# Kernel tuning notes

Hardware: AMD Instinct MI355X
Metric: run time of the kernel (lower is better)

Reference implementation:

```python
import jax, jax.numpy as jnp
import numpy as np

N_NODES = 50000
N_EDGES = 800000
IN_FEATS = 128
OUT_FEATS = 128
N_REL = 3


def setup_inputs() -> dict:
    key = jax.random.key(0)
    k1, k2, k3, k4, k5, k6 = jax.random.split(key, 6)
    feature = jax.random.normal(k1, (N_NODES, IN_FEATS), dtype=jnp.float32)
    # kaiming_uniform-ish scale for faithfulness of magnitude
    bound = float(np.sqrt(6.0 / IN_FEATS))
    weight = jax.random.uniform(k2, (N_REL, IN_FEATS, OUT_FEATS), dtype=jnp.float32,
                                minval=-bound, maxval=bound)
    norm = jax.random.uniform(k3, (N_EDGES,), dtype=jnp.float32)
    src = jax.random.randint(k4, (N_EDGES,), 0, N_NODES)
    dst = jax.random.randint(k5, (N_EDGES,), 0, N_NODES)
    rel_type = jax.random.randint(k6, (N_EDGES,), 0, N_REL)
    return {"feature": feature, "weight": weight, "norm": norm,
            "src": src, "dst": dst, "rel_type": rel_type}


def reference(feature, weight, norm, src, dst, rel_type):
    # Per-edge message: norm_e * (x[src_e] @ W[rel_type_e]).
    # Since there are only 3 relations, transform ALL nodes once per relation
    # (grouped GEMM: [3, N, in] x [3, in, out]) then gather the right
    # (relation, src) row per edge -- same math, avoids per-edge bmm.
    hr = jnp.einsum('ni,rio->rno', feature, weight)       # [3, N, out]
    msg = hr[rel_type, src] * norm[:, None]               # [E, out]
    # fn.sum reduce -> scatter-sum into destination nodes (zero if no in-edges)
    h = jax.ops.segment_sum(msg, dst, num_segments=feature.shape[0])  # [N, out]
    return jax.nn.relu(h)
```

## Files before the change

kernel.cpp:

```cpp
#include <hip/hip_runtime.h>
#include <stdint.h>

#define NFEAT  128
#define NREL   3

typedef short short8 __attribute__((ext_vector_type(8)));
typedef float f32x4  __attribute__((ext_vector_type(4)));

__device__ __forceinline__ uint32_t f2bf(float x) {
    uint32_t u = __builtin_bit_cast(uint32_t, x);
    uint32_t r = (u + 0x7FFFu + ((u >> 16) & 1u)) >> 16;
    return r & 0xFFFFu;
}
__device__ __forceinline__ float bf2f(uint32_t b) {
    uint32_t u = b << 16;
    return __builtin_bit_cast(float, u);
}

__global__ __launch_bounds__(256) void k_prep_w(
    const float* __restrict__ W, uint16_t* __restrict__ Wt, int* __restrict__ bincnt)
{
    const int tid = blockIdx.x * 256 + threadIdx.x;
    if (blockIdx.x == 0) bincnt[threadIdx.x] = 0;
    if (tid >= NREL * NFEAT * 16) return;
    const int k8 = tid & 15;
    const int o  = (tid >> 4) & 127;
    const int r  = tid >> 11;
    const float* Wr = W + (size_t)r * NFEAT * NFEAT;
    uint32_t pk[4];
    #pragma unroll
    for (int q = 0; q < 4; q++) {
        float lo = Wr[(size_t)(k8 * 8 + q * 2)     * NFEAT + o];
        float hi = Wr[(size_t)(k8 * 8 + q * 2 + 1) * NFEAT + o];
        pk[q] = f2bf(lo) | (f2bf(hi) << 16);
    }
    uint4 v = make_uint4(pk[0], pk[1], pk[2], pk[3]);
    *reinterpret_cast<uint4*>(&Wt[(size_t)r * NFEAT * NFEAT + (size_t)o * NFEAT + k8 * 8]) = v;
}

__global__ __launch_bounds__(256) void k_gemm_mfma(
    const float* __restrict__ feat, const uint16_t* __restrict__ Wt,
    uint16_t* __restrict__ hr, int N)
{
    __shared__ uint16_t ldsA[64 * 128];
    __shared__ uint16_t ldsB[128 * 128];

    const int t    = threadIdx.x;
    const int lane = t & 63;
    const int w    = t >> 6;
    const int n0   = blockIdx.x * 64;

    {
        const int kq = t & 15;
        const int rq = t >> 4;
        #pragma unroll
        for (int rr = 0; rr < 4; rr++) {
            const int row = rr * 16 + rq;
            const int n = n0 + row;
            uint4 pk = make_uint4(0, 0, 0, 0);
            if (n < N) {
                const float4* p = reinterpret_cast<const float4*>(&feat[(size_t)n * NFEAT + kq * 8]);
                float4 v0 = p[0], v1 = p[1];
                pk.x = f2bf(v0.x) | (f2bf(v0.y) << 16);
                pk.y = f2bf(v0.z) | (f2bf(v0.w) << 16);
                pk.z = f2bf(v1.x) | (f2bf(v1.y) << 16);
                pk.w = f2bf(v1.z) | (f2bf(v1.w) << 16);
            }
            uint32_t byte = (uint32_t)(row * 256 + kq * 16) ^ ((uint32_t)(row & 7) << 4);
            *reinterpret_cast<uint4*>(reinterpret_cast<char*>(ldsA) + byte) = pk;
        }
    }

    const int rowf = lane & 15;
    const int kb   = lane >> 4;

    for (int r = 0; r < NREL; r++) {
        {
            const int kq = t & 15;
            const int rq = t >> 4;
            const uint16_t* Wr = Wt + (size_t)r * NFEAT * NFEAT;
            #pragma unroll
            for (int rr = 0; rr < 8; rr++) {
                const int row = rr * 16 + rq;
                uint4 v = *reinterpret_cast<const uint4*>(&Wr[(size_t)row * NFEAT + kq * 8]);
                uint32_t byte = (uint32_t)(row * 256 + kq * 16) ^ ((uint32_t)(row & 7) << 4);
                *reinterpret_cast<uint4*>(reinterpret_cast<char*>(ldsB) + byte) = v;
            }
        }
        __syncthreads();

        short8 a[4];
        {
            const int row = w * 16 + rowf;
            #pragma unroll
            for (int ks = 0; ks < 4; ks++) {
                uint32_t byte = (uint32_t)(row * 256 + ks * 64 + kb * 16) ^ ((uint32_t)(row & 7) << 4);
                a[ks] = *reinterpret_cast<const short8*>(reinterpret_cast<char*>(ldsA) + byte);
            }
        }

        f32x4 acc[8];
        #pragma unroll
        for (int cf = 0; cf < 8; cf++) acc[cf] = (f32x4){0.f, 0.f, 0.f, 0.f};

        #pragma unroll
        for (int cf = 0; cf < 8; cf++) {
            const int col = cf * 16 + rowf;
            #pragma unroll
            for (int ks = 0; ks < 4; ks++) {
                uint32_t byte = (uint32_t)(col * 256 + ks * 64 + kb * 16) ^ ((uint32_t)(col & 7) << 4);
                short8 b = *reinterpret_cast<const short8*>(reinterpret_cast<char*>(ldsB) + byte);
                acc[cf] = __builtin_amdgcn_mfma_f32_16x16x32_bf16(a[ks], b, acc[cf], 0, 0, 0);
            }
        }

        #pragma unroll
        for (int cf = 0; cf < 8; cf++) {
            #pragma unroll
            for (int j = 0; j < 4; j++) {
                const int n = n0 + w * 16 + kb * 4 + j;
                if (n < N)
                    hr[((size_t)r * N + n) * NFEAT + cf * 16 + rowf] = (uint16_t)f2bf(acc[cf][j]);
            }
        }
        __syncthreads();
    }
}

__global__ __launch_bounds__(256) void k_binhist(
    const int* __restrict__ dst, int* __restrict__ bincnt, int E)
{
    __shared__ int h[256];
    const int t = threadIdx.x;
    h[t] = 0;
    __syncthreads();
    int e = blockIdx.x * 2048 + t;
    #pragma unroll
    for (int j = 0; j < 8; j++, e += 256)
        if (e < E) atomicAdd(&h[dst[e] >> 8], 1);
    __syncthreads();
    if (h[t]) atomicAdd(&bincnt[t], h[t]);
}

__global__ __launch_bounds__(256) void k_binscan(
    const int* __restrict__ bincnt, int* __restrict__ binoff,
    int* __restrict__ bincursor, int* __restrict__ offsets,
    int N, int E, int nbins)
{
    __shared__ int sm[256];
    const int t = threadIdx.x;
    int v = (t < nbins) ? bincnt[t] : 0;
    sm[t] = v;
    __syncthreads();
    for (int s = 1; s < 256; s <<= 1) {
        int a = (t >= s) ? sm[t - s] : 0;
        __syncthreads();
        sm[t] += a;
        __syncthreads();
    }
    int excl = sm[t] - v;
    if (t < nbins) { binoff[t] = excl; bincursor[t] = excl; }
    if (t == 0) { binoff[nbins] = E; offsets[N] = E; }
}

__global__ __launch_bounds__(256) void k_binfill(
    const int* __restrict__ dst, const int* __restrict__ src,
    const int* __restrict__ rel, const float* __restrict__ norm,
    int* __restrict__ bincursor, uint2* __restrict__ binbuf, int E)
{
    __shared__ int hist[256];
    __shared__ int base[256];
    __shared__ int rank[256];
    const int t = threadIdx.x;
    const int e0 = blockIdx.x * 2048;

    hist[t] = 0;
    __syncthreads();

    int myBin[8], myDl[8];
    #pragma unroll
    for (int j = 0; j < 8; j++) {
        int e = e0 + t + j * 256;
        int b = -1, dl = 0;
        if (e < E) {
            int d = dst[e];
            b = d >> 8;
            dl = d & 255;
            atomicAdd(&hist[b], 1);
        }
        myBin[j] = b;
        myDl[j] = dl;
    }
    __syncthreads();

    int h = hist[t];
    if (h > 0) base[t] = atomicAdd(&bincursor[t], h);
    rank[t] = 0;
    __syncthreads();

    #pragma unroll
    for (int j = 0; j < 8; j++) {
        int e = e0 + t + j * 256;
        if (myBin[j] >= 0) {
            int p = base[myBin[j]] + atomicAdd(&rank[myBin[j]], 1);
            uint32_t px = (uint32_t)src[e] | ((uint32_t)rel[e] << 16) | ((uint32_t)myDl[j] << 18);
            binbuf[p] = make_uint2(px, __builtin_bit_cast(uint32_t, norm[e]));
        }
    }
}

__global__ __launch_bounds__(256) void k_binsort(
    const uint2* __restrict__ binbuf, const int* __restrict__ binoff,
    uint2* __restrict__ meta, int* __restrict__ offsets, int N)
{
    __shared__ int sm[256];
    __shared__ int cur[256];
    const int b = blockIdx.x;
    const int t = threadIdx.x;
    const int base = binoff[b];
    const int cnt  = binoff[b + 1] - base;

    sm[t] = 0;
    __syncthreads();
    for (int i = t; i < cnt; i += 256) {
        uint2 r = binbuf[base + i];
        atomicAdd(&sm[(r.x >> 18) & 255], 1);
    }
    __syncthreads();
    int v = sm[t];
    __syncthreads();
    sm[t] = v;
    __syncthreads();
    for (int s = 1; s < 256; s <<= 1) {
        int a = (t >= s) ? sm[t - s] : 0;
        __syncthreads();
        sm[t] += a;
        __syncthreads();
    }
    int excl = sm[t] - v;
    int n = b * 256 + t;
    if (n < N) offsets[n] = base + excl;
    cur[t] = excl;
    __syncthreads();

    for (int i = t; i < cnt; i += 256) {
        uint2 r = binbuf[base + i];
        int dl = (r.x >> 18) & 255;
        int p = atomicAdd(&cur[dl], 1);
        meta[base + p] = make_uint2(r.x & 0x3FFFFu, r.y);
    }
}

__global__ __launch_bounds__(256) void k_aggregate(
    const uint16_t* __restrict__ hr, const int* __restrict__ offsets,
    const uint2* __restrict__ meta, float* __restrict__ out, int N)
{
    const int wid  = threadIdx.x >> 6;
    const int lane = threadIdx.x & 63;
    const int n = blockIdx.x * 4 + wid;
    if (n >= N) return;

    const int start = offsets[n];
    const int end   = offsets[n + 1];
    const int c = lane * 2;

    float a0 = 0.f, a1 = 0.f, b0 = 0.f, b1 = 0.f;
    int idx = start;

    for (; idx + 7 < end; idx += 8) {
        uint2 m[8];
        #pragma unroll
        for (int j = 0; j < 8; j++) m[j] = meta[idx + j];
        uint32_t v[8];
        #pragma unroll
        for (int j = 0; j < 8; j++)
            v[j] = *reinterpret_cast<const uint32_t*>(
                &hr[((size_t)(m[j].x >> 16) * N + (m[j].x & 0xFFFFu)) * NFEAT + c]);
        #pragma unroll
        for (int j = 0; j < 8; j += 2) {
            float w0 = __builtin_bit_cast(float, m[j].y);
            float w1 = __builtin_bit_cast(float, m[j + 1].y);
            a0 += w0 * bf2f(v[j] & 0xFFFFu);     a1 += w0 * bf2f(v[j] >> 16);
            b0 += w1 * bf2f(v[j + 1] & 0xFFFFu); b1 += w1 * bf2f(v[j + 1] >> 16);
        }
    }
    for (; idx + 3 < end; idx += 4) {
        uint2 m[4];
        #pragma unroll
        for (int j = 0; j < 4; j++) m[j] = meta[idx + j];
        uint32_t v[4];
        #pragma unroll
        for (int j = 0; j < 4; j++)
            v[j] = *reinterpret_cast<const uint32_t*>(
                &hr[((size_t)(m[j].x >> 16) * N + (m[j].x & 0xFFFFu)) * NFEAT + c]);
        #pragma unroll
        for (int j = 0; j < 4; j += 2) {
            float w0 = __builtin_bit_cast(float, m[j].y);
            float w1 = __builtin_bit_cast(float, m[j + 1].y);
            a0 += w0 * bf2f(v[j] & 0xFFFFu);     a1 += w0 * bf2f(v[j] >> 16);
            b0 += w1 * bf2f(v[j + 1] & 0xFFFFu); b1 += w1 * bf2f(v[j + 1] >> 16);
        }
    }
    for (; idx < end; idx++) {
        uint2 m = meta[idx];
        uint32_t v = *reinterpret_cast<const uint32_t*>(
            &hr[((size_t)(m.x >> 16) * N + (m.x & 0xFFFFu)) * NFEAT + c]);
        float wgt = __builtin_bit_cast(float, m.y);
        a0 += wgt * bf2f(v & 0xFFFFu);
        a1 += wgt * bf2f(v >> 16);
    }

    float2 o;
    o.x = fmaxf(a0 + b0, 0.f);
    o.y = fmaxf(a1 + b1, 0.f);
    *reinterpret_cast<float2*>(&out[(size_t)n * NFEAT + c]) = o;
}

extern "C" void kernel_launch(void* const* d_in, const int* in_sizes, int n_in,
                              void* d_out, int out_size, void* d_ws, size_t ws_size,
                              hipStream_t stream)
{
    const float* feat = (const float*)d_in[0];
    const float* W    = (const float*)d_in[1];
    const float* norm = (const float*)d_in[2];
    const int*   src  = (const int*)d_in[3];
    const int*   dst  = (const int*)d_in[4];
    const int*   rel  = (const int*)d_in[5];
    float* out = (float*)d_out;

    const int N = in_sizes[0] / NFEAT;
    const int E = in_sizes[2];
    const int NBINS = (N + 255) / 256;
    const int HB = (E + 2047) / 2048;

    char* ws = (char*)d_ws;
    size_t off = 0;
    auto alloc = [&](size_t bytes) -> char* {
        char* p = ws + off;
        off += (bytes + 63) & ~(size_t)63;
        return p;
    };
    uint16_t* hr    = (uint16_t*)alloc((size_t)NREL * N * NFEAT * 2);
    uint16_t* Wt    = (uint16_t*)alloc((size_t)NREL * NFEAT * NFEAT * 2);
    int* bincnt     = (int*)alloc(256 * 4);
    int* binoff     = (int*)alloc(257 * 4);
    int* bincursor  = (int*)alloc(256 * 4);
    int* offsets    = (int*)alloc((size_t)(N + 1) * 4);
    uint2* meta     = (uint2*)alloc((size_t)E * 8);
    (void)ws_size;

    uint2* binbuf = (uint2*)d_out;

    k_prep_w<<<(NREL * NFEAT * 16 + 255) / 256, 256, 0, stream>>>(W, Wt, bincnt);
    k_gemm_mfma<<<(N + 63) / 64, 256, 0, stream>>>(feat, Wt, hr, N);
    k_binhist<<<HB, 256, 0, stream>>>(dst, bincnt, E);
    k_binscan<<<1, 256, 0, stream>>>(bincnt, binoff, bincursor, offsets, N, E, NBINS);
    k_binfill<<<HB, 256, 0, stream>>>(dst, src, rel, norm, bincursor, binbuf, E);
    k_binsort<<<NBINS, 256, 0, stream>>>(binbuf, binoff, meta, offsets, N);
    k_aggregate<<<(N + 3) / 4, 256, 0, stream>>>(hr, offsets, meta, out, N);
}
```

Measured before the change: 107.4 us.

## Aggregate raw features per relation before the weight GEMM

```diff
diff --git a/kernel.cpp b/kernel.cpp
--- a/kernel.cpp
+++ b/kernel.cpp
@@ -17,150 +17,83 @@
     return __builtin_bit_cast(float, u);
 }
 
-__global__ __launch_bounds__(256) void k_prep_w(
-    const float* __restrict__ W, uint16_t* __restrict__ Wt, int* __restrict__ bincnt)
-{
-    const int tid = blockIdx.x * 256 + threadIdx.x;
-    if (blockIdx.x == 0) bincnt[threadIdx.x] = 0;
-    if (tid >= NREL * NFEAT * 16) return;
-    const int k8 = tid & 15;
-    const int o  = (tid >> 4) & 127;
-    const int r  = tid >> 11;
-    const float* Wr = W + (size_t)r * NFEAT * NFEAT;
-    uint32_t pk[4];
-    #pragma unroll
-    for (int q = 0; q < 4; q++) {
-        float lo = Wr[(size_t)(k8 * 8 + q * 2)     * NFEAT + o];
-        float hi = Wr[(size_t)(k8 * 8 + q * 2 + 1) * NFEAT + o];
-        pk[q] = f2bf(lo) | (f2bf(hi) << 16);
-    }
-    uint4 v = make_uint4(pk[0], pk[1], pk[2], pk[3]);
-    *reinterpret_cast<uint4*>(&Wt[(size_t)r * NFEAT * NFEAT + (size_t)o * NFEAT + k8 * 8]) = v;
-}
-
-__global__ __launch_bounds__(256) void k_gemm_mfma(
-    const float* __restrict__ feat, const uint16_t* __restrict__ Wt,
-    uint16_t* __restrict__ hr, int N)
-{
-    __shared__ uint16_t ldsA[64 * 128];
-    __shared__ uint16_t ldsB[128 * 128];
-
-    const int t    = threadIdx.x;
-    const int lane = t & 63;
-    const int w    = t >> 6;
-    const int n0   = blockIdx.x * 64;
-
-    {
-        const int kq = t & 15;
-        const int rq = t >> 4;
-        #pragma unroll
-        for (int rr = 0; rr < 4; rr++) {
-            const int row = rr * 16 + rq;
-            const int n = n0 + row;
-            uint4 pk = make_uint4(0, 0, 0, 0);
-            if (n < N) {
-                const float4* p = reinterpret_cast<const float4*>(&feat[(size_t)n * NFEAT + kq * 8]);
-                float4 v0 = p[0], v1 = p[1];
-                pk.x = f2bf(v0.x) | (f2bf(v0.y) << 16);
-                pk.y = f2bf(v0.z) | (f2bf(v0.w) << 16);
-                pk.z = f2bf(v1.x) | (f2bf(v1.y) << 16);
-                pk.w = f2bf(v1.z) | (f2bf(v1.w) << 16);
-            }
-            uint32_t byte = (uint32_t)(row * 256 + kq * 16) ^ ((uint32_t)(row & 7) << 4);
-            *reinterpret_cast<uint4*>(reinterpret_cast<char*>(ldsA) + byte) = pk;
-        }
-    }
-
-    const int rowf = lane & 15;
-    const int kb   = lane >> 4;
-
-    for (int r = 0; r < NREL; r++) {
-        {
-            const int kq = t & 15;
-            const int rq = t >> 4;
-            const uint16_t* Wr = Wt + (size_t)r * NFEAT * NFEAT;
-            #pragma unroll
-            for (int rr = 0; rr < 8; rr++) {
-                const int row = rr * 16 + rq;
-                uint4 v = *reinterpret_cast<const uint4*>(&Wr[(size_t)row * NFEAT + kq * 8]);
-                uint32_t byte = (uint32_t)(row * 256 + kq * 16) ^ ((uint32_t)(row & 7) << 4);
-                *reinterpret_cast<uint4*>(reinterpret_cast<char*>(ldsB) + byte) = v;
-            }
-        }
-        __syncthreads();
-
-        short8 a[4];
-        {
-            const int row = w * 16 + rowf;
-            #pragma unroll
-            for (int ks = 0; ks < 4; ks++) {
-                uint32_t byte = (uint32_t)(row * 256 + ks * 64 + kb * 16) ^ ((uint32_t)(row & 7) << 4);
-                a[ks] = *reinterpret_cast<const short8*>(reinterpret_cast<char*>(ldsA) + byte);
-            }
-        }
-
-        f32x4 acc[8];
-        #pragma unroll
-        for (int cf = 0; cf < 8; cf++) acc[cf] = (f32x4){0.f, 0.f, 0.f, 0.f};
-
-        #pragma unroll
-        for (int cf = 0; cf < 8; cf++) {
-            const int col = cf * 16 + rowf;
-            #pragma unroll
-            for (int ks = 0; ks < 4; ks++) {
-                uint32_t byte = (uint32_t)(col * 256 + ks * 64 + kb * 16) ^ ((uint32_t)(col & 7) << 4);
-                short8 b = *reinterpret_cast<const short8*>(reinterpret_cast<char*>(ldsB) + byte);
-                acc[cf] = __builtin_amdgcn_mfma_f32_16x16x32_bf16(a[ks], b, acc[cf], 0, 0, 0);
-            }
-        }
-
-        #pragma unroll
-        for (int cf = 0; cf < 8; cf++) {
-            #pragma unroll
-            for (int j = 0; j < 4; j++) {
-                const int n = n0 + w * 16 + kb * 4 + j;
-                if (n < N)
-                    hr[((size_t)r * N + n) * NFEAT + cf * 16 + rowf] = (uint16_t)f2bf(acc[cf][j]);
-            }
-        }
-        __syncthreads();
-    }
-}
-
-__global__ __launch_bounds__(256) void k_binhist(
-    const int* __restrict__ dst, int* __restrict__ bincnt, int E)
+__global__ __launch_bounds__(256) void k_prep(
+    const float* __restrict__ feat, const float* __restrict__ W,
+    const int* __restrict__ dst,
+    uint16_t* __restrict__ featb, uint16_t* __restrict__ Wt,
+    int* __restrict__ binpartial,
+    int N, int E, int FBn, int WBn)
 {
     __shared__ int h[256];
     const int t = threadIdx.x;
+    const int bid = blockIdx.x;
+
+    if (bid < FBn) {
+        const int i = bid * 256 + t;
+        if (i < N * (NFEAT / 8)) {
+            const float4* p = reinterpret_cast<const float4*>(feat + (size_t)i * 8);
+            float4 v0 = p[0], v1 = p[1];
+            uint4 pk;
+            pk.x = f2bf(v0.x) | (f2bf(v0.y) << 16);
+            pk.y = f2bf(v0.z) | (f2bf(v0.w) << 16);
+            pk.z = f2bf(v1.x) | (f2bf(v1.y) << 16);
+            pk.w = f2bf(v1.z) | (f2bf(v1.w) << 16);
+            *reinterpret_cast<uint4*>(featb + (size_t)i * 8) = pk;
+        }
+        return;
+    }
+    if (bid < FBn + WBn) {
+        const int tid = (bid - FBn) * 256 + t;
+        if (tid < NREL * NFEAT * 16) {
+            const int k8 = tid & 15;
+            const int o  = (tid >> 4) & 127;
+            const int r  = tid >> 11;
+            const float* Wr = W + (size_t)r * NFEAT * NFEAT;
+            uint32_t pk[4];
+            #pragma unroll
+            for (int q = 0; q < 4; q++) {
+                float lo = Wr[(size_t)(k8 * 8 + q * 2)     * NFEAT + o];
+                float hi = Wr[(size_t)(k8 * 8 + q * 2 + 1) * NFEAT + o];
+                pk[q] = f2bf(lo) | (f2bf(hi) << 16);
+            }
+            uint4 v = make_uint4(pk[0], pk[1], pk[2], pk[3]);
+            *reinterpret_cast<uint4*>(&Wt[(size_t)r * NFEAT * NFEAT + (size_t)o * NFEAT + k8 * 8]) = v;
+        }
+        return;
+    }
     h[t] = 0;
     __syncthreads();
-    int e = blockIdx.x * 2048 + t;
+    const int hb = bid - FBn - WBn;
+    int e = hb * 2048 + t;
     #pragma unroll
     for (int j = 0; j < 8; j++, e += 256)
         if (e < E) atomicAdd(&h[dst[e] >> 8], 1);
     __syncthreads();
-    if (h[t]) atomicAdd(&bincnt[t], h[t]);
+    binpartial[hb * 256 + t] = h[t];
 }
 
 __global__ __launch_bounds__(256) void k_binscan(
-    const int* __restrict__ bincnt, int* __restrict__ binoff,
+    const int* __restrict__ binpartial, int* __restrict__ binoff,
     int* __restrict__ bincursor, int* __restrict__ offsets,
-    int N, int E, int nbins)
+    int N, int E, int nparts)
 {
     __shared__ int sm[256];
     const int t = threadIdx.x;
-    int v = (t < nbins) ? bincnt[t] : 0;
-    sm[t] = v;
-    __syncthreads();
-    for (int s = 1; s < 256; s <<= 1) {
-        int a = (t >= s) ? sm[t - s] : 0;
+    int s = 0;
+    #pragma unroll 4
+    for (int b = 0; b < nparts; b++) s += binpartial[b * 256 + t];
+    sm[t] = s;
+    __syncthreads();
+    for (int st = 1; st < 256; st <<= 1) {
+        int a = (t >= st) ? sm[t - st] : 0;
         __syncthreads();
         sm[t] += a;
         __syncthreads();
     }
-    int excl = sm[t] - v;
-    if (t < nbins) { binoff[t] = excl; bincursor[t] = excl; }
-    if (t == 0) { binoff[nbins] = E; offsets[N] = E; }
+    int excl = sm[t] - s;
+    binoff[t] = excl;
+    bincursor[t] = excl;
+    if (t == 0) { binoff[256] = E; offsets[N] = E; }
 }
 
 __global__ __launch_bounds__(256) void k_binfill(
@@ -251,9 +184,9 @@
     }
 }
 
-__global__ __launch_bounds__(256) void k_aggregate(
-    const uint16_t* __restrict__ hr, const int* __restrict__ offsets,
-    const uint2* __restrict__ meta, float* __restrict__ out, int N)
+__global__ __launch_bounds__(256) void k_agg_raw(
+    const uint16_t* __restrict__ featb, const int* __restrict__ offsets,
+    const uint2* __restrict__ meta, uint16_t* __restrict__ aggb, int N)
 {
     const int wid  = threadIdx.x >> 6;
     const int lane = threadIdx.x & 63;
@@ -264,26 +197,9 @@
     const int end   = offsets[n + 1];
     const int c = lane * 2;
 
-    float a0 = 0.f, a1 = 0.f, b0 = 0.f, b1 = 0.f;
+    float a00 = 0.f, a01 = 0.f, a10 = 0.f, a11 = 0.f, a20 = 0.f, a21 = 0.f;
     int idx = start;
 
-    for (; idx + 7 < end; idx += 8) {
-        uint2 m[8];
-        #pragma unroll
-        for (int j = 0; j < 8; j++) m[j] = meta[idx + j];
-        uint32_t v[8];
-        #pragma unroll
-        for (int j = 0; j < 8; j++)
-            v[j] = *reinterpret_cast<const uint32_t*>(
-                &hr[((size_t)(m[j].x >> 16) * N + (m[j].x & 0xFFFFu)) * NFEAT + c]);
-        #pragma unroll
-        for (int j = 0; j < 8; j += 2) {
-            float w0 = __builtin_bit_cast(float, m[j].y);
-            float w1 = __builtin_bit_cast(float, m[j + 1].y);
-            a0 += w0 * bf2f(v[j] & 0xFFFFu);     a1 += w0 * bf2f(v[j] >> 16);
-            b0 += w1 * bf2f(v[j + 1] & 0xFFFFu); b1 += w1 * bf2f(v[j + 1] >> 16);
-        }
-    }
     for (; idx + 3 < end; idx += 4) {
         uint2 m[4];
         #pragma unroll
@@ -292,28 +208,114 @@
         #pragma unroll
         for (int j = 0; j < 4; j++)
             v[j] = *reinterpret_cast<const uint32_t*>(
-                &hr[((size_t)(m[j].x >> 16) * N + (m[j].x & 0xFFFFu)) * NFEAT + c]);
-        #pragma unroll
-        for (int j = 0; j < 4; j += 2) {
-            float w0 = __builtin_bit_cast(float, m[j].y);
-            float w1 = __builtin_bit_cast(float, m[j + 1].y);
-            a0 += w0 * bf2f(v[j] & 0xFFFFu);     a1 += w0 * bf2f(v[j] >> 16);
-            b0 += w1 * bf2f(v[j + 1] & 0xFFFFu); b1 += w1 * bf2f(v[j + 1] >> 16);
+                &featb[(size_t)(m[j].x & 0xFFFFu) * NFEAT + c]);
+        #pragma unroll
+        for (int j = 0; j < 4; j++) {
+            float wgt = __builtin_bit_cast(float, m[j].y);
+            float lo = wgt * bf2f(v[j] & 0xFFFFu);
+            float hi = wgt * bf2f(v[j] >> 16);
+            uint32_t r = m[j].x >> 16;
+            if (r == 0)      { a00 += lo; a01 += hi; }
+            else if (r == 1) { a10 += lo; a11 += hi; }
+            else             { a20 += lo; a21 += hi; }
         }
     }
     for (; idx < end; idx++) {
         uint2 m = meta[idx];
         uint32_t v = *reinterpret_cast<const uint32_t*>(
-            &hr[((size_t)(m.x >> 16) * N + (m.x & 0xFFFFu)) * NFEAT + c]);
+            &featb[(size_t)(m.x & 0xFFFFu) * NFEAT + c]);
         float wgt = __builtin_bit_cast(float, m.y);
-        a0 += wgt * bf2f(v & 0xFFFFu);
-        a1 += wgt * bf2f(v >> 16);
-    }
-
-    float2 o;
-    o.x = fmaxf(a0 + b0, 0.f);
-    o.y = fmaxf(a1 + b1, 0.f);
-    *reinterpret_cast<float2*>(&out[(size_t)n * NFEAT + c]) = o;
+        float lo = wgt * bf2f(v & 0xFFFFu);
+        float hi = wgt * bf2f(v >> 16);
+        uint32_t r = m.x >> 16;
+        if (r == 0)      { a00 += lo; a01 += hi; }
+        else if (r == 1) { a10 += lo; a11 += hi; }
+        else             { a20 += lo; a21 += hi; }
+    }
+
+    const size_t base = (size_t)n * (NREL * NFEAT) + c;
+    *reinterpret_cast<uint32_t*>(&aggb[base])             = f2bf(a00) | (f2bf(a01) << 16);
+    *reinterpret_cast<uint32_t*>(&aggb[base + NFEAT])     = f2bf(a10) | (f2bf(a11) << 16);
+    *reinterpret_cast<uint32_t*>(&aggb[base + 2 * NFEAT]) = f2bf(a20) | (f2bf(a21) << 16);
+}
+
+__global__ __launch_bounds__(256) void k_gemm_out(
+    const uint16_t* __restrict__ aggb, const uint16_t* __restrict__ Wt,
+    float* __restrict__ out, int N)
+{
+    __shared__ uint16_t ldsA[64 * 128];
+    __shared__ uint16_t ldsB[128 * 128];
+
+    const int t    = threadIdx.x;
+    const int lane = t & 63;
+    const int w    = t >> 6;
+    const int n0   = blockIdx.x * 64;
+
+    const int rowf = lane & 15;
+    const int kb   = lane >> 4;
+
+    f32x4 acc[8];
+    #pragma unroll
+    for (int cf = 0; cf < 8; cf++) acc[cf] = (f32x4){0.f, 0.f, 0.f, 0.f};
+
+    for (int r = 0; r < NREL; r++) {
+        if (r) __syncthreads();
+        {
+            const int kq = t & 15;
+            const int rq = t >> 4;
+            #pragma unroll
+            for (int rr = 0; rr < 4; rr++) {
+                const int row = rr * 16 + rq;
+                const int n = n0 + row;
+                uint4 v = make_uint4(0, 0, 0, 0);
+                if (n < N)
+                    v = *reinterpret_cast<const uint4*>(
+                        &aggb[((size_t)n * NREL + r) * NFEAT + kq * 8]);
+                uint32_t byte = (uint32_t)(row * 256 + kq * 16) ^ ((uint32_t)(row & 7) << 4);
+                *reinterpret_cast<uint4*>(reinterpret_cast<char*>(ldsA) + byte) = v;
+            }
+            const uint16_t* Wr = Wt + (size_t)r * NFEAT * NFEAT;
+            #pragma unroll
+            for (int rr = 0; rr < 8; rr++) {
+                const int row = rr * 16 + rq;
+                uint4 v = *reinterpret_cast<const uint4*>(&Wr[(size_t)row * NFEAT + kq * 8]);
+                uint32_t byte = (uint32_t)(row * 256 + kq * 16) ^ ((uint32_t)(row & 7) << 4);
+                *reinterpret_cast<uint4*>(reinterpret_cast<char*>(ldsB) + byte) = v;
+            }
+        }
+        __syncthreads();
+
+        short8 a[4];
+        {
+            const int row = w * 16 + rowf;
+            #pragma unroll
+            for (int ks = 0; ks < 4; ks++) {
+                uint32_t byte = (uint32_t)(row * 256 + ks * 64 + kb * 16) ^ ((uint32_t)(row & 7) << 4);
+                a[ks] = *reinterpret_cast<const short8*>(reinterpret_cast<char*>(ldsA) + byte);
+            }
+        }
+
+        #pragma unroll
+        for (int cf = 0; cf < 8; cf++) {
+            const int col = cf * 16 + rowf;
+            #pragma unroll
+            for (int ks = 0; ks < 4; ks++) {
+                uint32_t byte = (uint32_t)(col * 256 + ks * 64 + kb * 16) ^ ((uint32_t)(col & 7) << 4);
+                short8 b = *reinterpret_cast<const short8*>(reinterpret_cast<char*>(ldsB) + byte);
+                acc[cf] = __builtin_amdgcn_mfma_f32_16x16x32_bf16(a[ks], b, acc[cf], 0, 0, 0);
+            }
+        }
+    }
+
+    #pragma unroll
+    for (int cf = 0; cf < 8; cf++) {
+        #pragma unroll
+        for (int j = 0; j < 4; j++) {
+            const int n = n0 + w * 16 + kb * 4 + j;
+            if (n < N)
+                out[(size_t)n * NFEAT + cf * 16 + rowf] = fmaxf(acc[cf][j], 0.f);
+        }
+    }
 }
 
 extern "C" void kernel_launch(void* const* d_in, const int* in_sizes, int n_in,
@@ -331,7 +333,9 @@
     const int N = in_sizes[0] / NFEAT;
     const int E = in_sizes[2];
     const int NBINS = (N + 255) / 256;
-    const int HB = (E + 2047) / 2048;
+    const int HB  = (E + 2047) / 2048;
+    const int FBn = (N * (NFEAT / 8) + 255) / 256;
+    const int WBn = (NREL * NFEAT * 16 + 255) / 256;
 
     char* ws = (char*)d_ws;
     size_t off = 0;
@@ -340,22 +344,22 @@
         off += (bytes + 63) & ~(size_t)63;
         return p;
     };
-    uint16_t* hr    = (uint16_t*)alloc((size_t)NREL * N * NFEAT * 2);
-    uint16_t* Wt    = (uint16_t*)alloc((size_t)NREL * NFEAT * NFEAT * 2);
-    int* bincnt     = (int*)alloc(256 * 4);
-    int* binoff     = (int*)alloc(257 * 4);
-    int* bincursor  = (int*)alloc(256 * 4);
-    int* offsets    = (int*)alloc((size_t)(N + 1) * 4);
-    uint2* meta     = (uint2*)alloc((size_t)E * 8);
+    uint16_t* aggb   = (uint16_t*)alloc((size_t)N * NREL * NFEAT * 2);
+    uint16_t* Wt     = (uint16_t*)alloc((size_t)NREL * NFEAT * NFEAT * 2);
+    int* binpartial  = (int*)alloc((size_t)HB * 256 * 4);
+    int* binoff      = (int*)alloc(257 * 4);
+    int* bincursor   = (int*)alloc(256 * 4);
+    int* offsets     = (int*)alloc((size_t)(N + 1) * 4);
+    uint2* meta      = (uint2*)alloc((size_t)E * 8);
     (void)ws_size;
 
-    uint2* binbuf = (uint2*)d_out;
-
-    k_prep_w<<<(NREL * NFEAT * 16 + 255) / 256, 256, 0, stream>>>(W, Wt, bincnt);
-    k_gemm_mfma<<<(N + 63) / 64, 256, 0, stream>>>(feat, Wt, hr, N);
-    k_binhist<<<HB, 256, 0, stream>>>(dst, bincnt, E);
-    k_binscan<<<1, 256, 0, stream>>>(bincnt, binoff, bincursor, offsets, N, E, NBINS);
+    uint2* binbuf   = (uint2*)d_out;
+    uint16_t* featb = (uint16_t*)((char*)d_out + (8u << 20));
+
+    k_prep<<<FBn + WBn + HB, 256, 0, stream>>>(feat, W, dst, featb, Wt, binpartial, N, E, FBn, WBn);
+    k_binscan<<<1, 256, 0, stream>>>(binpartial, binoff, bincursor, offsets, N, E, HB);
     k_binfill<<<HB, 256, 0, stream>>>(dst, src, rel, norm, bincursor, binbuf, E);
     k_binsort<<<NBINS, 256, 0, stream>>>(binbuf, binoff, meta, offsets, N);
-    k_aggregate<<<(N + 3) / 4, 256, 0, stream>>>(hr, offsets, meta, out, N);
-}
+    k_agg_raw<<<(N + 3) / 4, 256, 0, stream>>>(featb, offsets, meta, aggb, N);
+    k_gemm_out<<<(N + 63) / 64, 256, 0, stream>>>(aggb, Wt, out, N);
+}
```

Measured after the change: 125.6 us. 16.9% more time.

## Merge weight prep with histogram, use per-block partials, precompute gather row index

Applied to the files above, without the earlier changes.

```diff
diff --git a/kernel.cpp b/kernel.cpp
--- a/kernel.cpp
+++ b/kernel.cpp
@@ -12,30 +12,50 @@
     uint32_t r = (u + 0x7FFFu + ((u >> 16) & 1u)) >> 16;
     return r & 0xFFFFu;
 }
-__device__ __forceinline__ float bf2f(uint32_t b) {
-    uint32_t u = b << 16;
-    return __builtin_bit_cast(float, u);
-}
-
-__global__ __launch_bounds__(256) void k_prep_w(
-    const float* __restrict__ W, uint16_t* __restrict__ Wt, int* __restrict__ bincnt)
-{
-    const int tid = blockIdx.x * 256 + threadIdx.x;
-    if (blockIdx.x == 0) bincnt[threadIdx.x] = 0;
-    if (tid >= NREL * NFEAT * 16) return;
-    const int k8 = tid & 15;
-    const int o  = (tid >> 4) & 127;
-    const int r  = tid >> 11;
-    const float* Wr = W + (size_t)r * NFEAT * NFEAT;
-    uint32_t pk[4];
+__device__ __forceinline__ float bf_lo(uint32_t v) {
+    return __builtin_bit_cast(float, v << 16);
+}
+__device__ __forceinline__ float bf_hi(uint32_t v) {
+    return __builtin_bit_cast(float, v & 0xFFFF0000u);
+}
+
+__global__ __launch_bounds__(256) void k_prep(
+    const float* __restrict__ W, const int* __restrict__ dst,
+    uint16_t* __restrict__ Wt, int* __restrict__ binpartial,
+    int E, int WBn)
+{
+    __shared__ int h[256];
+    const int t = threadIdx.x;
+    const int bid = blockIdx.x;
+
+    if (bid < WBn) {
+        const int tid = bid * 256 + t;
+        if (tid < NREL * NFEAT * 16) {
+            const int k8 = tid & 15;
+            const int o  = (tid >> 4) & 127;
+            const int r  = tid >> 11;
+            const float* Wr = W + (size_t)r * NFEAT * NFEAT;
+            uint32_t pk[4];
+            #pragma unroll
+            for (int q = 0; q < 4; q++) {
+                float lo = Wr[(size_t)(k8 * 8 + q * 2)     * NFEAT + o];
+                float hi = Wr[(size_t)(k8 * 8 + q * 2 + 1) * NFEAT + o];
+                pk[q] = f2bf(lo) | (f2bf(hi) << 16);
+            }
+            uint4 v = make_uint4(pk[0], pk[1], pk[2], pk[3]);
+            *reinterpret_cast<uint4*>(&Wt[(size_t)r * NFEAT * NFEAT + (size_t)o * NFEAT + k8 * 8]) = v;
+        }
+        return;
+    }
+    h[t] = 0;
+    __syncthreads();
+    const int hb = bid - WBn;
+    int e = hb * 2048 + t;
     #pragma unroll
-    for (int q = 0; q < 4; q++) {
-        float lo = Wr[(size_t)(k8 * 8 + q * 2)     * NFEAT + o];
-        float hi = Wr[(size_t)(k8 * 8 + q * 2 + 1) * NFEAT + o];
-        pk[q] = f2bf(lo) | (f2bf(hi) << 16);
-    }
-    uint4 v = make_uint4(pk[0], pk[1], pk[2], pk[3]);
-    *reinterpret_cast<uint4*>(&Wt[(size_t)r * NFEAT * NFEAT + (size_t)o * NFEAT + k8 * 8]) = v;
+    for (int j = 0; j < 8; j++, e += 256)
+        if (e < E) atomicAdd(&h[dst[e] >> 8], 1);
+    __syncthreads();
+    binpartial[hb * 256 + t] = h[t];
 }
 
 __global__ __launch_bounds__(256) void k_gemm_mfma(
@@ -127,46 +147,34 @@
     }
 }
 
-__global__ __launch_bounds__(256) void k_binhist(
-    const int* __restrict__ dst, int* __restrict__ bincnt, int E)
-{
-    __shared__ int h[256];
-    const int t = threadIdx.x;
-    h[t] = 0;
-    __syncthreads();
-    int e = blockIdx.x * 2048 + t;
-    #pragma unroll
-    for (int j = 0; j < 8; j++, e += 256)
-        if (e < E) atomicAdd(&h[dst[e] >> 8], 1);
-    __syncthreads();
-    if (h[t]) atomicAdd(&bincnt[t], h[t]);
-}
-
 __global__ __launch_bounds__(256) void k_binscan(
-    const int* __restrict__ bincnt, int* __restrict__ binoff,
+    const int* __restrict__ binpartial, int* __restrict__ binoff,
     int* __restrict__ bincursor, int* __restrict__ offsets,
-    int N, int E, int nbins)
+    int N, int E, int nparts)
 {
     __shared__ int sm[256];
     const int t = threadIdx.x;
-    int v = (t < nbins) ? bincnt[t] : 0;
-    sm[t] = v;
-    __syncthreads();
-    for (int s = 1; s < 256; s <<= 1) {
-        int a = (t >= s) ? sm[t - s] : 0;
+    int s = 0;
+    #pragma unroll 4
+    for (int b = 0; b < nparts; b++) s += binpartial[b * 256 + t];
+    sm[t] = s;
+    __syncthreads();
+    for (int st = 1; st < 256; st <<= 1) {
+        int a = (t >= st) ? sm[t - st] : 0;
         __syncthreads();
         sm[t] += a;
         __syncthreads();
     }
-    int excl = sm[t] - v;
-    if (t < nbins) { binoff[t] = excl; bincursor[t] = excl; }
-    if (t == 0) { binoff[nbins] = E; offsets[N] = E; }
+    int excl = sm[t] - s;
+    binoff[t] = excl;
+    bincursor[t] = excl;
+    if (t == 0) { binoff[256] = E; offsets[N] = E; }
 }
 
 __global__ __launch_bounds__(256) void k_binfill(
     const int* __restrict__ dst, const int* __restrict__ src,
     const int* __restrict__ rel, const float* __restrict__ norm,
-    int* __restrict__ bincursor, uint2* __restrict__ binbuf, int E)
+    int* __restrict__ bincursor, uint2* __restrict__ binbuf, int N, int E)
 {
     __shared__ int hist[256];
     __shared__ int base[256];
@@ -203,7 +211,8 @@
         int e = e0 + t + j * 256;
         if (myBin[j] >= 0) {
             int p = base[myBin[j]] + atomicAdd(&rank[myBin[j]], 1);
-            uint32_t px = (uint32_t)src[e] | ((uint32_t)rel[e] << 16) | ((uint32_t)myDl[j] << 18);
+            uint32_t rowidx = (uint32_t)(rel[e] * N + src[e]);
+            uint32_t px = rowidx | ((uint32_t)myDl[j] << 18);
             binbuf[p] = make_uint2(px, __builtin_bit_cast(uint32_t, norm[e]));
         }
     }
@@ -262,7 +271,7 @@
 
     const int start = offsets[n];
     const int end   = offsets[n + 1];
-    const int c = lane * 2;
+    const char* hrb = reinterpret_cast<const char*>(hr) + lane * 4;
 
     float a0 = 0.f, a1 = 0.f, b0 = 0.f, b1 = 0.f;
     int idx = start;
@@ -274,14 +283,13 @@
         uint32_t v[8];
         #pragma unroll
         for (int j = 0; j < 8; j++)
-            v[j] = *reinterpret_cast<const uint32_t*>(
-                &hr[((size_t)(m[j].x >> 16) * N + (m[j].x & 0xFFFFu)) * NFEAT + c]);
+            v[j] = *reinterpret_cast<const uint32_t*>(hrb + ((size_t)m[j].x << 8));
         #pragma unroll
         for (int j = 0; j < 8; j += 2) {
             float w0 = __builtin_bit_cast(float, m[j].y);
             float w1 = __builtin_bit_cast(float, m[j + 1].y);
-            a0 += w0 * bf2f(v[j] & 0xFFFFu);     a1 += w0 * bf2f(v[j] >> 16);
-            b0 += w1 * bf2f(v[j + 1] & 0xFFFFu); b1 += w1 * bf2f(v[j + 1] >> 16);
+            a0 += w0 * bf_lo(v[j]);     a1 += w0 * bf_hi(v[j]);
+            b0 += w1 * bf_lo(v[j + 1]); b1 += w1 * bf_hi(v[j + 1]);
         }
     }
     for (; idx + 3 < end; idx += 4) {
@@ -291,29 +299,27 @@
         uint32_t v[4];
         #pragma unroll
         for (int j = 0; j < 4; j++)
-            v[j] = *reinterpret_cast<const uint32_t*>(
-                &hr[((size_t)(m[j].x >> 16) * N + (m[j].x & 0xFFFFu)) * NFEAT + c]);
+            v[j] = *reinterpret_cast<const uint32_t*>(hrb + ((size_t)m[j].x << 8));
         #pragma unroll
         for (int j = 0; j < 4; j += 2) {
             float w0 = __builtin_bit_cast(float, m[j].y);
             float w1 = __builtin_bit_cast(float, m[j + 1].y);
-            a0 += w0 * bf2f(v[j] & 0xFFFFu);     a1 += w0 * bf2f(v[j] >> 16);
-            b0 += w1 * bf2f(v[j + 1] & 0xFFFFu); b1 += w1 * bf2f(v[j + 1] >> 16);
+            a0 += w0 * bf_lo(v[j]);     a1 += w0 * bf_hi(v[j]);
+            b0 += w1 * bf_lo(v[j + 1]); b1 += w1 * bf_hi(v[j + 1]);
         }
     }
     for (; idx < end; idx++) {
         uint2 m = meta[idx];
-        uint32_t v = *reinterpret_cast<const uint32_t*>(
-            &hr[((size_t)(m.x >> 16) * N + (m.x & 0xFFFFu)) * NFEAT + c]);
+        uint32_t v = *reinterpret_cast<const uint32_t*>(hrb + ((size_t)m.x << 8));
         float wgt = __builtin_bit_cast(float, m.y);
-        a0 += wgt * bf2f(v & 0xFFFFu);
-        a1 += wgt * bf2f(v >> 16);
+        a0 += wgt * bf_lo(v);
+        a1 += wgt * bf_hi(v);
     }
 
     float2 o;
     o.x = fmaxf(a0 + b0, 0.f);
     o.y = fmaxf(a1 + b1, 0.f);
-    *reinterpret_cast<float2*>(&out[(size_t)n * NFEAT + c]) = o;
+    *reinterpret_cast<float2*>(&out[(size_t)n * NFEAT + lane * 2]) = o;
 }
 
 extern "C" void kernel_launch(void* const* d_in, const int* in_sizes, int n_in,
@@ -331,7 +337,8 @@
     const int N = in_sizes[0] / NFEAT;
     const int E = in_sizes[2];
     const int NBINS = (N + 255) / 256;
-    const int HB = (E + 2047) / 2048;
+    const int HB  = (E + 2047) / 2048;
+    const int WBn = (NREL * NFEAT * 16 + 255) / 256;
 
     char* ws = (char*)d_ws;
     size_t off = 0;
@@ -340,22 +347,21 @@
         off += (bytes + 63) & ~(size_t)63;
         return p;
     };
-    uint16_t* hr    = (uint16_t*)alloc((size_t)NREL * N * NFEAT * 2);
-    uint16_t* Wt    = (uint16_t*)alloc((size_t)NREL * NFEAT * NFEAT * 2);
-    int* bincnt     = (int*)alloc(256 * 4);
-    int* binoff     = (int*)alloc(257 * 4);
-    int* bincursor  = (int*)alloc(256 * 4);
-    int* offsets    = (int*)alloc((size_t)(N + 1) * 4);
-    uint2* meta     = (uint2*)alloc((size_t)E * 8);
+    uint16_t* hr     = (uint16_t*)alloc((size_t)NREL * N * NFEAT * 2);
+    uint16_t* Wt     = (uint16_t*)alloc((size_t)NREL * NFEAT * NFEAT * 2);
+    int* binpartial  = (int*)alloc((size_t)HB * 256 * 4);
+    int* binoff      = (int*)alloc(257 * 4);
+    int* bincursor   = (int*)alloc(256 * 4);
+    int* offsets     = (int*)alloc((size_t)(N + 1) * 4);
+    uint2* meta      = (uint2*)alloc((size_t)E * 8);
     (void)ws_size;
 
     uint2* binbuf = (uint2*)d_out;
 
-    k_prep_w<<<(NREL * NFEAT * 16 + 255) / 256, 256, 0, stream>>>(W, Wt, bincnt);
+    k_prep<<<WBn + HB, 256, 0, stream>>>(W, dst, Wt, binpartial, E, WBn);
     k_gemm_mfma<<<(N + 63) / 64, 256, 0, stream>>>(feat, Wt, hr, N);
-    k_binhist<<<HB, 256, 0, stream>>>(dst, bincnt, E);
-    k_binscan<<<1, 256, 0, stream>>>(bincnt, binoff, bincursor, offsets, N, E, NBINS);
-    k_binfill<<<HB, 256, 0, stream>>>(dst, src, rel, norm, bincursor, binbuf, E);
+    k_binscan<<<1, 256, 0, stream>>>(binpartial, binoff, bincursor, offsets, N, E, HB);
+    k_binfill<<<HB, 256, 0, stream>>>(dst, src, rel, norm, bincursor, binbuf, N, E);
     k_binsort<<<NBINS, 256, 0, stream>>>(binbuf, binoff, meta, offsets, N);
     k_aggregate<<<(N + 3) / 4, 256, 0, stream>>>(hr, offsets, meta, out, N);
 }
```

After: 115.2 us. 1.07x slower.
